# Optimization experiments

Measured on AMD Instinct MI355X. Metric: run time of the kernel, lower is better.

Reference implementation:

```python
import jax, jax.numpy as jnp
import numpy as np
from jax import lax

V, D, L = 32000, 1024, 8
HQ, HKV, HD = 16, 4, 64          # head_dim = D // HQ
H = int(2.6875 * D)              # SwiGLU hidden = 2752
B, S = 2, 1024
WINDOW, GEVERY = 256, 4
EPS, BASE = 1e-6, 10000.0
STD = 0.02


def setup_inputs() -> dict:
    key = jax.random.key(0)
    ks = jax.random.split(key, 10)
    return {
        "idx": jax.random.randint(ks[0], (B, S), 0, V, dtype=jnp.int32),
        "emb": jax.random.normal(ks[1], (V, D), jnp.float32) * STD,
        "Wq": jax.random.normal(ks[2], (L, D, HQ * HD), jnp.float32) * STD,
        "Wk": jax.random.normal(ks[3], (L, D, HKV * HD), jnp.float32) * STD,
        "Wv": jax.random.normal(ks[4], (L, D, HKV * HD), jnp.float32) * STD,
        "Wo": jax.random.normal(ks[5], (L, HQ * HD, D), jnp.float32) * (STD / np.sqrt(2 * L)).astype(np.float32),
        "w1": jax.random.normal(ks[6], (L, D, H), jnp.float32) * STD,
        "w3": jax.random.normal(ks[7], (L, D, H), jnp.float32) * STD,
        "w2": jax.random.normal(ks[8], (L, H, D), jnp.float32) * (STD / np.sqrt(2 * L)).astype(np.float32),
        "n1": jnp.ones((L, D), jnp.float32),
        "n2": jnp.ones((L, D), jnp.float32),
        "nf": jnp.ones((D,), jnp.float32),
    }


def _rmsnorm(x, w):
    return x * lax.rsqrt(jnp.mean(x * x, axis=-1, keepdims=True) + EPS) * w


def _rope(x, cos, sin):
    # x: [B,S,h,HD]; pairs (even, odd) rotated by complex multiply with e^{i*theta}
    x2 = x.reshape(*x.shape[:-1], HD // 2, 2)
    x0, x1 = x2[..., 0], x2[..., 1]
    r0 = x0 * cos - x1 * sin
    r1 = x0 * sin + x1 * cos
    return jnp.stack([r0, r1], axis=-1).reshape(x.shape)


def _forward(idx, emb, Wq, Wk, Wv, Wo, w1, w3, w2, n1, n2, nf):
    # RoPE cache (RoPECache._build_cache)
    inv_freq = 1.0 / (BASE ** (jnp.arange(0, HD, 2, dtype=jnp.float32) / HD))
    t = jnp.arange(S, dtype=jnp.float32)
    freqs = t[:, None] * inv_freq[None, :]                      # [S, HD//2]
    cos = jnp.cos(freqs)[None, :, None, :]                      # [1,S,1,HD//2]
    sin = jnp.sin(freqs)[None, :, None, :]

    # masks: global causal and sliding-window causal (additive, 0 / -inf)
    pos = jnp.arange(S)
    causal = pos[None, :] <= pos[:, None]
    local = causal & ((pos[:, None] - pos[None, :]) < WINDOW)
    neg_inf = jnp.float32(-jnp.inf)
    gmask = jnp.where(causal, 0.0, neg_inf).astype(jnp.float32)
    lmask = jnp.where(local, 0.0, neg_inf).astype(jnp.float32)
    use_global = ((jnp.arange(L) + 1) % GEVERY) == 0            # [L] bool

    scale = 1.0 / (HD ** 0.5)
    rep = HQ // HKV

    def block(x, p):
        wq, wk, wv, wo, W1, W3, W2, g1, g2, ug = p
        h = _rmsnorm(x, g1)
        q = (h @ wq).reshape(B, S, HQ, HD)
        k = (h @ wk).reshape(B, S, HKV, HD)
        v = (h @ wv).reshape(B, S, HKV, HD)
        q = _rope(q, cos, sin)
        k = _rope(k, cos, sin)
        k = jnp.repeat(k, rep, axis=2)                          # GQA: expand KV heads
        v = jnp.repeat(v, rep, axis=2)
        mask = jnp.where(ug, gmask, lmask)
        sc = jnp.einsum('bqhd,bkhd->bhqk', q, k) * scale + mask
        attn = jax.nn.softmax(sc, axis=-1)
        o = jnp.einsum('bhqk,bkhd->bqhd', attn, v).reshape(B, S, HQ * HD)
        x = x + o @ wo
        h2 = _rmsnorm(x, g2)
        x = x + (jax.nn.silu(h2 @ W1) * (h2 @ W3)) @ W2
        return x, None

    x = emb[idx]                                                # token embedding
    x, _ = lax.scan(block, x, (Wq, Wk, Wv, Wo, w1, w3, w2, n1, n2, use_global))
    logits = _rmsnorm(x, nf) @ emb.T                            # tied lm_head
    return logits


def reference(idx, emb, Wq, Wk, Wv, Wo, w1, w3, w2, n1, n2, nf):
    return _forward(idx, emb, Wq, Wk, Wv, Wo, w1, w3, w2, n1, n2, nf)
```

## Files before the change

kernel.cpp:

```cpp
#include <hip/hip_runtime.h>

#define V_ 32000
#define D_ 1024
#define L_ 8
#define HQ_ 16
#define HKV_ 4
#define HD_ 64
#define H_ 2752
#define B_ 2
#define S_ 1024
#define BS_ 2048
#define WINDOW_ 256

typedef float f32x4 __attribute__((ext_vector_type(4)));
typedef short s16x8 __attribute__((ext_vector_type(8)));
typedef unsigned short u16;

__device__ __forceinline__ u16 f2b(float f) {
  union { float f; unsigned u; } a; a.f = f;
  return (u16)((a.u + 0x7fffu + ((a.u >> 16) & 1u)) >> 16);
}
__device__ __forceinline__ float b2f(u16 b) {
  union { unsigned u; float f; } a; a.u = ((unsigned)b) << 16; return a.f;
}

__device__ __forceinline__ void gload_lds16(const void* g, void* l) {
  __builtin_amdgcn_global_load_lds(
      (const __attribute__((address_space(1))) void*)(unsigned long long)(uintptr_t)g,
      (__attribute__((address_space(3))) void*)(unsigned int)(uintptr_t)l,
      16, 0, 0);
}

__global__ void k_cvt(const float* __restrict__ src, u16* __restrict__ dst, long n4) {
  long i = (long)blockIdx.x * blockDim.x + threadIdx.x;
  if (i >= n4) return;
  float4 v = ((const float4*)src)[i];
  ushort4 o; o.x = f2b(v.x); o.y = f2b(v.y); o.z = f2b(v.z); o.w = f2b(v.w);
  ((ushort4*)dst)[i] = o;
}

struct TMat { const float* src; u16* dst; int R, C, t0; };
struct T7 { TMat m[7]; };

__global__ void k_transpose7(T7 P) {
  __shared__ float tile[32][33];
  int bid = blockIdx.x;
  int mi = 0;
#pragma unroll
  for (int i = 1; i < 7; ++i) if (bid >= P.m[i].t0) mi = i;
  TMat mm = P.m[mi];
  int tl = bid - mm.t0;
  int ct = mm.C >> 5;
  int tr = tl / ct, tc = tl - tr * ct;
  int r0 = tr << 5, c0 = tc << 5;
  int tx = threadIdx.x & 31, ty = threadIdx.x >> 5;
#pragma unroll
  for (int j = 0; j < 4; ++j)
    tile[ty + j * 8][tx] = mm.src[(size_t)(r0 + ty + j * 8) * mm.C + c0 + tx];
  __syncthreads();
#pragma unroll
  for (int j = 0; j < 4; ++j)
    mm.dst[(size_t)(c0 + ty + j * 8) * mm.R + r0 + tx] = f2b(tile[tx][ty + j * 8]);
}

__global__ void k_embed(const int* __restrict__ idx, const float* __restrict__ emb,
                        float* __restrict__ x) {
  int t = blockIdx.x;
  int token = idx[t];
  const float4* s = (const float4*)(emb + (size_t)token * D_);
  float4* d = (float4*)(x + (size_t)t * D_);
  d[threadIdx.x] = s[threadIdx.x];
}

__global__ void k_rmsnorm(const float* __restrict__ x, const float* __restrict__ w,
                          u16* __restrict__ out) {
  int row = blockIdx.x, tid = threadIdx.x;
  float4 v = ((const float4*)(x + (size_t)row * D_))[tid];
  float ss = v.x * v.x + v.y * v.y + v.z * v.z + v.w * v.w;
#pragma unroll
  for (int m = 1; m < 64; m <<= 1) ss += __shfl_xor(ss, m, 64);
  __shared__ float red[4];
  if ((tid & 63) == 0) red[tid >> 6] = ss;
  __syncthreads();
  float tot = red[0] + red[1] + red[2] + red[3];
  float rs = rsqrtf(tot * (1.0f / D_) + 1e-6f);
  float4 wv = ((const float4*)w)[tid];
  ushort4 o;
  o.x = f2b(v.x * rs * wv.x); o.y = f2b(v.y * rs * wv.y);
  o.z = f2b(v.z * rs * wv.z); o.w = f2b(v.w * rs * wv.w);
  ((ushort4*)(out + (size_t)row * D_))[tid] = o;
}

__global__ void k_ropetab(float* __restrict__ cosT, float* __restrict__ sinT) {
  int i = blockIdx.x * blockDim.x + threadIdx.x;
  int s = i >> 5, d = i & 31;
  float inv = __expf(-((float)(2 * d) / (float)HD_) * logf(10000.0f));
  float f = (float)s * inv;
  cosT[i] = cosf(f); sinT[i] = sinf(f);
}

__global__ void k_rope(const float* __restrict__ qkvf, const float* __restrict__ cosT,
                       const float* __restrict__ sinT, u16* __restrict__ qh,
                       u16* __restrict__ kh) {
  int t = blockIdx.x;
  int b = t >> 10, s = t & (S_ - 1);
  int tid = threadIdx.x;
  const float* row = qkvf + (size_t)t * 1536;
  for (int p = tid; p < 512; p += 256) {
    int hh = p >> 5, d = p & 31;
    float x0 = row[hh * 64 + 2 * d], x1 = row[hh * 64 + 2 * d + 1];
    float c = cosT[s * 32 + d], sn = sinT[s * 32 + d];
    size_t o = ((size_t)(b * HQ_ + hh) * S_ + s) * HD_ + 2 * d;
    qh[o] = f2b(x0 * c - x1 * sn);
    qh[o + 1] = f2b(x0 * sn + x1 * c);
  }
  if (tid < 128) {
    int hh = tid >> 5, d = tid & 31;
    float x0 = row[1024 + hh * 64 + 2 * d], x1 = row[1024 + hh * 64 + 2 * d + 1];
    float c = cosT[s * 32 + d], sn = sinT[s * 32 + d];
    size_t o = ((size_t)(b * HKV_ + hh) * S_ + s) * HD_ + 2 * d;
    kh[o] = f2b(x0 * c - x1 * sn);
    kh[o + 1] = f2b(x0 * sn + x1 * c);
  }
}

__global__ void k_vtrans(const float* __restrict__ qkvf, u16* __restrict__ vth) {
  __shared__ float tile[32][65];
  const int s0 = blockIdx.x << 5, hh = blockIdx.y, b = blockIdx.z;
  const int tx = threadIdx.x & 63, ty = threadIdx.x >> 6;
#pragma unroll
  for (int j = 0; j < 8; ++j) {
    int sl = j * 4 + ty;
    tile[sl][tx] = qkvf[(size_t)((b << 10) + s0 + sl) * 1536 + 1280 + hh * 64 + tx];
  }
  __syncthreads();
  const int sx = threadIdx.x & 31, dr = threadIdx.x >> 5;
#pragma unroll
  for (int j = 0; j < 8; ++j) {
    int d = j * 8 + dr;
    vth[((size_t)((b * HKV_ + hh) << 6) + d) * S_ + s0 + sx] = f2b(tile[sx][d]);
  }
}

template <int EPI>
__global__ __launch_bounds__(256) void k_gemm(const u16* __restrict__ A,
                                              const u16* __restrict__ BT,
                                              void* __restrict__ Cp, int M, int N, int K,
                                              int ldc) {
  (void)M; (void)N;
  __shared__ u16 As[3][4096];
  __shared__ u16 Bs[3][4096];
  const int tid = threadIdx.x;
  const int lane = tid & 63, wid = tid >> 6;
  const int lin = blockIdx.y * 16 + blockIdx.x;
  const int cpx = (gridDim.x * gridDim.y) >> 3;
  const int swz = (lin & 7) * cpx + (lin >> 3);
  const int m0 = (swz & 15) << 7, n0 = (swz >> 4) << 7;
  const int wm = (wid >> 1) << 6, wn = (wid & 1) << 6;
  const int fr = lane & 15, fg = lane >> 4;

  f32x4 acc[4][4] = {};

  const int srow = (wid << 4) + (lane >> 2);
  const int scol = ((lane & 3) - ((lane >> 3) & 3)) & 3;
  const u16* ga = A + (size_t)(m0 + srow) * K + (scol << 3);
  const u16* gb = BT + (size_t)(n0 + srow) * K + (scol << 3);
  const int cb = wid << 9;

  auto stage = [&](int buf, int k0) {
    u16* la = &As[buf][cb];
    u16* lb = &Bs[buf][cb];
    gload_lds16(ga + k0, la);
    gload_lds16(ga + (size_t)64 * K + k0, la + 2048);
    gload_lds16(gb + k0, lb);
    gload_lds16(gb + (size_t)64 * K + k0, lb + 2048);
  };

  const int nk = K >> 5;
  stage(0, 0);
  stage(1, 32);

  const int ab = (wid >> 1) << 2, bb = (wid & 1) << 2;
  const int foff = (fr << 5) + ((((fg + (fr >> 1)) & 3)) << 3);
  int cur = 0;
  for (int t = 0; t < nk; ++t) {
    if (t + 2 < nk) {
      int nb = cur + 2; if (nb >= 3) nb -= 3;
      stage(nb, (t + 2) << 5);
      asm volatile("s_waitcnt vmcnt(8)" ::: "memory");
    } else if (t + 2 == nk) {
      asm volatile("s_waitcnt vmcnt(4)" ::: "memory");
    } else {
      asm volatile("s_waitcnt vmcnt(0)" ::: "memory");
    }
    __builtin_amdgcn_s_barrier();
    s16x8 af[4], bq[4];
#pragma unroll
    for (int i = 0; i < 4; ++i) {
      af[i] = *(const s16x8*)(&As[cur][((ab + i) << 9) + foff]);
      bq[i] = *(const s16x8*)(&Bs[cur][((bb + i) << 9) + foff]);
    }
#pragma unroll
    for (int mi = 0; mi < 4; ++mi)
#pragma unroll
      for (int ni = 0; ni < 4; ++ni)
        acc[mi][ni] = __builtin_amdgcn_mfma_f32_16x16x32_bf16(af[mi], bq[ni], acc[mi][ni], 0, 0, 0);
    __builtin_amdgcn_s_barrier();
    if (++cur == 3) cur = 0;
  }

#pragma unroll
  for (int mi = 0; mi < 4; ++mi) {
#pragma unroll
    for (int ni = 0; ni < 4; ++ni) {
#pragma unroll
      for (int r = 0; r < 4; ++r) {
        int row = m0 + wm + mi * 16 + fg * 4 + r;
        int col = n0 + wn + ni * 16 + fr;
        size_t off = (size_t)row * ldc + col;
        float v = acc[mi][ni][r];
        if (EPI == 0) ((float*)Cp)[off] = v;
        else if (EPI == 1) ((float*)Cp)[off] += v;
        else ((u16*)Cp)[off] = f2b(v);
      }
    }
  }
}

template <int EPI>
__global__ __launch_bounds__(256, 2) void k_gemm2(const u16* __restrict__ A,
                                                  const u16* __restrict__ BT,
                                                  void* __restrict__ Cp, int K, int ldc) {
  __shared__ u16 As[3][8192];
  __shared__ u16 Bs[3][4096];
  const int tid = threadIdx.x;
  const int lane = tid & 63, wid = tid >> 6;
  const int lin = blockIdx.y * gridDim.x + blockIdx.x;
  const int cpx = (gridDim.x * gridDim.y) >> 3;
  const int swz = (lin & 7) * cpx + (lin >> 3);
  const int m0 = (swz & 7) << 8, n0 = (swz >> 3) << 7;
  const int fr = lane & 15, fg = lane >> 4;

  f32x4 acc[4][8] = {};

  const int srow = lane >> 2;
  const int scol = ((lane & 3) - ((lane >> 3) & 3)) & 3;
  const u16* ga = A + (size_t)(m0 + (wid << 6) + srow) * K + (scol << 3);
  const u16* gb = BT + (size_t)(n0 + (wid << 5) + srow) * K + (scol << 3);
  const int cba = wid << 11;
  const int cbb = wid << 10;

  auto stage = [&](int buf, int k0) {
    u16* la = &As[buf][cba];
    u16* lb = &Bs[buf][cbb];
    gload_lds16(ga + k0, la);
    gload_lds16(ga + (size_t)16 * K + k0, la + 512);
    gload_lds16(ga + (size_t)32 * K + k0, la + 1024);
    gload_lds16(ga + (size_t)48 * K + k0, la + 1536);
    gload_lds16(gb + k0, lb);
    gload_lds16(gb + (size_t)16 * K + k0, lb + 512);
  };

  const int nk = K >> 5;
  stage(0, 0);
  stage(1, 32);

  const int foff = (fr << 5) + ((((fg + (fr >> 1)) & 3)) << 3);
  int cur = 0;
  for (int t = 0; t < nk; ++t) {
    if (t + 2 < nk) {
      int nb = cur + 2; if (nb >= 3) nb -= 3;
      stage(nb, (t + 2) << 5);
      asm volatile("s_waitcnt vmcnt(12)" ::: "memory");
    } else if (t + 2 == nk) {
      asm volatile("s_waitcnt vmcnt(6)" ::: "memory");
    } else {
      asm volatile("s_waitcnt vmcnt(0)" ::: "memory");
    }
    __builtin_amdgcn_s_barrier();
    s16x8 af[4], bq[8];
#pragma unroll
    for (int i = 0; i < 4; ++i)
      af[i] = *(const s16x8*)(&As[cur][(((wid << 2) + i) << 9) + foff]);
#pragma unroll
    for (int j = 0; j < 8; ++j)
      bq[j] = *(const s16x8*)(&Bs[cur][(j << 9) + foff]);
#pragma unroll
    for (int mi = 0; mi < 4; ++mi)
#pragma unroll
      for (int ni = 0; ni < 8; ++ni)
        acc[mi][ni] = __builtin_amdgcn_mfma_f32_16x16x32_bf16(af[mi], bq[ni], acc[mi][ni], 0, 0, 0);
    __builtin_amdgcn_s_barrier();
    if (++cur == 3) cur = 0;
  }

#pragma unroll
  for (int mi = 0; mi < 4; ++mi) {
#pragma unroll
    for (int ni = 0; ni < 8; ++ni) {
#pragma unroll
      for (int r = 0; r < 4; ++r) {
        int row = m0 + (wid << 6) + mi * 16 + fg * 4 + r;
        int col = n0 + ni * 16 + fr;
        size_t off = (size_t)row * ldc + col;
        float v = acc[mi][ni][r];
        if (EPI == 0) ((float*)Cp)[off] = v;
        else if (EPI == 1) ((float*)Cp)[off] += v;
        else ((u16*)Cp)[off] = f2b(v);
      }
    }
  }
}

__global__ __launch_bounds__(256) void k_attn(const u16* __restrict__ qh,
                                              const u16* __restrict__ kh,
                                              const u16* __restrict__ vth,
                                              u16* __restrict__ attno, int isGlobal) {
  __shared__ u16 pb[4][512];
  const int qblk = blockIdx.x, hq = blockIdx.y, b = blockIdx.z;
  const int lane = threadIdx.x & 63, wid = threadIdx.x >> 6;
  const int fr = lane & 15, fg = lane >> 4;
  const int q0 = (qblk << 6) + (wid << 4);
  const int hk = hq >> 2;
  const u16* Q = qh + ((size_t)(b * HQ_ + hq) * S_) * HD_;
  const u16* Kh = kh + ((size_t)(b * HKV_ + hk) * S_) * HD_;
  const u16* VT = vth + ((size_t)(b * HKV_ + hk) * HD_) * S_;
  u16* pbuf = pb[wid];

  const s16x8 aq0 = *(const s16x8*)(Q + (q0 + fr) * HD_ + fg * 8);
  const s16x8 aq1 = *(const s16x8*)(Q + (q0 + fr) * HD_ + 32 + fg * 8);

  f32x4 o0 = {}, o1 = {}, o2 = {}, o3 = {};
  float m[4], l[4];
#pragma unroll
  for (int r = 0; r < 4; ++r) { m[r] = -1e30f; l[r] = 0.0f; }

  int kt0 = 0;
  if (!isGlobal) { int lo = q0 - (WINDOW_ - 1); if (lo > 0) kt0 = lo & ~31; }
  const int ktend = q0 + 16;

  for (int kt = kt0; kt < ktend; kt += 32) {
    f32x4 sc0 = {}, sc1 = {};
    {
      s16x8 b0 = *(const s16x8*)(Kh + (kt + fr) * HD_ + fg * 8);
      s16x8 b1 = *(const s16x8*)(Kh + (kt + fr) * HD_ + 32 + fg * 8);
      sc0 = __builtin_amdgcn_mfma_f32_16x16x32_bf16(aq0, b0, sc0, 0, 0, 0);
      sc0 = __builtin_amdgcn_mfma_f32_16x16x32_bf16(aq1, b1, sc0, 0, 0, 0);
      s16x8 c0 = *(const s16x8*)(Kh + (kt + 16 + fr) * HD_ + fg * 8);
      s16x8 c1 = *(const s16x8*)(Kh + (kt + 16 + fr) * HD_ + 32 + fg * 8);
      sc1 = __builtin_amdgcn_mfma_f32_16x16x32_bf16(aq0, c0, sc1, 0, 0, 0);
      sc1 = __builtin_amdgcn_mfma_f32_16x16x32_bf16(aq1, c1, sc1, 0, 0, 0);
    }
#pragma unroll
    for (int r = 0; r < 4; ++r) {
      int row = q0 + fg * 4 + r;
      int col0 = kt + fr, col1 = kt + 16 + fr;
      bool v0 = (col0 <= row) && (isGlobal || (row - col0) < WINDOW_);
      bool v1 = (col1 <= row) && (isGlobal || (row - col1) < WINDOW_);
      float s0 = v0 ? sc0[r] * 0.125f : -1e30f;
      float s1 = v1 ? sc1[r] * 0.125f : -1e30f;
      float t = fmaxf(s0, s1);
#pragma unroll
      for (int msk = 1; msk < 16; msk <<= 1) t = fmaxf(t, __shfl_xor(t, msk, 16));
      float mn = fmaxf(m[r], t);
      float fsc = __expf(m[r] - mn);
      m[r] = mn;
      float p0 = v0 ? __expf(s0 - mn) : 0.0f;
      float p1 = v1 ? __expf(s1 - mn) : 0.0f;
      float ps = p0 + p1;
#pragma unroll
      for (int msk = 1; msk < 16; msk <<= 1) ps += __shfl_xor(ps, msk, 16);
      l[r] = l[r] * fsc + ps;
      o0[r] *= fsc; o1[r] *= fsc; o2[r] *= fsc; o3[r] *= fsc;
      pbuf[(fg * 4 + r) * 32 + fr] = f2b(p0);
      pbuf[(fg * 4 + r) * 32 + 16 + fr] = f2b(p1);
    }
    s16x8 ap = *(const s16x8*)(pbuf + fr * 32 + fg * 8);
    {
      s16x8 bv0 = *(const s16x8*)(VT + (size_t)(0 + fr) * S_ + kt + fg * 8);
      o0 = __builtin_amdgcn_mfma_f32_16x16x32_bf16(ap, bv0, o0, 0, 0, 0);
      s16x8 bv1 = *(const s16x8*)(VT + (size_t)(16 + fr) * S_ + kt + fg * 8);
      o1 = __builtin_amdgcn_mfma_f32_16x16x32_bf16(ap, bv1, o1, 0, 0, 0);
      s16x8 bv2 = *(const s16x8*)(VT + (size_t)(32 + fr) * S_ + kt + fg * 8);
      o2 = __builtin_amdgcn_mfma_f32_16x16x32_bf16(ap, bv2, o2, 0, 0, 0);
      s16x8 bv3 = *(const s16x8*)(VT + (size_t)(48 + fr) * S_ + kt + fg * 8);
      o3 = __builtin_amdgcn_mfma_f32_16x16x32_bf16(ap, bv3, o3, 0, 0, 0);
    }
  }

#pragma unroll
  for (int r = 0; r < 4; ++r) {
    int row = q0 + fg * 4 + r;
    float inv = 1.0f / l[r];
    size_t base = ((size_t)b * S_ + row) * (HQ_ * HD_) + hq * HD_;
    attno[base + fr] = f2b(o0[r] * inv);
    attno[base + 16 + fr] = f2b(o1[r] * inv);
    attno[base + 32 + fr] = f2b(o2[r] * inv);
    attno[base + 48 + fr] = f2b(o3[r] * inv);
  }
}

__global__ void k_silu(const u16* __restrict__ h13, u16* __restrict__ g) {
  long c = (long)blockIdx.x * 256 + threadIdx.x;
  int t = (int)(c / 688);
  int j = (int)(c - (long)t * 688) * 4;
  const u16* a = h13 + (size_t)t * 5504 + j;
  ushort4 av = *(const ushort4*)a;
  ushort4 bv = *(const ushort4*)(a + 2752);
  ushort4 ov;
  {
    float x0 = b2f(av.x), y0 = b2f(bv.x);
    ov.x = f2b(x0 / (1.0f + __expf(-x0)) * y0);
  }
  {
    float x0 = b2f(av.y), y0 = b2f(bv.y);
    ov.y = f2b(x0 / (1.0f + __expf(-x0)) * y0);
  }
  {
    float x0 = b2f(av.z), y0 = b2f(bv.z);
    ov.z = f2b(x0 / (1.0f + __expf(-x0)) * y0);
  }
  {
    float x0 = b2f(av.w), y0 = b2f(bv.w);
    ov.w = f2b(x0 / (1.0f + __expf(-x0)) * y0);
  }
  *(ushort4*)(g + (size_t)t * 2752 + j) = ov;
}

extern "C" void kernel_launch(void* const* d_in, const int* in_sizes, int n_in,
                              void* d_out, int out_size, void* d_ws, size_t ws_size,
                              hipStream_t stream) {
  (void)in_sizes; (void)n_in; (void)out_size; (void)ws_size;
  const int* idx = (const int*)d_in[0];
  const float* emb = (const float*)d_in[1];
  const float* Wq = (const float*)d_in[2];
  const float* Wk = (const float*)d_in[3];
  const float* Wv = (const float*)d_in[4];
  const float* Wo = (const float*)d_in[5];
  const float* w1 = (const float*)d_in[6];
  const float* w3 = (const float*)d_in[7];
  const float* w2 = (const float*)d_in[8];
  const float* n1 = (const float*)d_in[9];
  const float* n2 = (const float*)d_in[10];
  const float* nf = (const float*)d_in[11];
  float* out = (float*)d_out;

  char* p = (char*)d_ws;
  auto carve = [&](size_t bytes) {
    char* q = p;
    p += (bytes + 255) & ~(size_t)255;
    return (void*)q;
  };
  float* x = (float*)carve((size_t)BS_ * D_ * 4);
  u16* h = (u16*)carve((size_t)BS_ * D_ * 2);
  float* qkvf = (float*)carve((size_t)BS_ * 1536 * 4);
  u16* qh = (u16*)carve((size_t)B_ * HQ_ * S_ * HD_ * 2);
  u16* khb = (u16*)carve((size_t)B_ * HKV_ * S_ * HD_ * 2);
  u16* vth = (u16*)carve((size_t)B_ * HKV_ * HD_ * S_ * 2);
  u16* attno = (u16*)carve((size_t)BS_ * D_ * 2);
  u16* h13 = (u16*)carve((size_t)BS_ * 5504 * 2);
  u16* g = (u16*)carve((size_t)BS_ * H_ * 2);
  u16* wT = (u16*)carve((size_t)11075584 * 2);
  float* cosT = (float*)carve((size_t)S_ * 32 * 4);
  float* sinT = (float*)carve((size_t)S_ * 32 * 4);
  u16* embb = (u16*)carve((size_t)V_ * D_ * 2);

  k_cvt<<<V_ * D_ / 4 / 256, 256, 0, stream>>>(emb, embb, (long)V_ * D_ / 4);
  k_ropetab<<<S_ * 32 / 256, 256, 0, stream>>>(cosT, sinT);
  k_embed<<<BS_, 256, 0, stream>>>(idx, emb, x);

  for (int l = 0; l < L_; ++l) {
    T7 t7;
    t7.m[0] = { Wq + (size_t)l * D_ * 1024, wT, D_, 1024, 0 };
    t7.m[1] = { Wk + (size_t)l * D_ * 256, wT + 1048576, D_, 256, 1024 };
    t7.m[2] = { Wv + (size_t)l * D_ * 256, wT + 1310720, D_, 256, 1280 };
    t7.m[3] = { Wo + (size_t)l * 1024 * D_, wT + 1572864, 1024, D_, 1536 };
    t7.m[4] = { w1 + (size_t)l * D_ * H_, wT + 2621440, D_, H_, 2560 };
    t7.m[5] = { w3 + (size_t)l * D_ * H_, wT + 5439488, D_, H_, 5312 };
    t7.m[6] = { w2 + (size_t)l * H_ * D_, wT + 8257536, H_, D_, 8064 };
    k_transpose7<<<10816, 256, 0, stream>>>(t7);

    k_rmsnorm<<<BS_, 256, 0, stream>>>(x, n1 + (size_t)l * D_, h);
    k_gemm<0><<<dim3(16, 12), 256, 0, stream>>>(h, wT, qkvf, BS_, 1536, 1024, 1536);
    k_rope<<<BS_, 256, 0, stream>>>(qkvf, cosT, sinT, qh, khb);
    k_vtrans<<<dim3(32, HKV_, B_), 256, 0, stream>>>(qkvf, vth);
    int ig = ((l + 1) % 4) == 0;
    k_attn<<<dim3(16, HQ_, B_), 256, 0, stream>>>(qh, khb, vth, attno, ig);
    k_gemm<1><<<dim3(16, 8), 256, 0, stream>>>(attno, wT + 1572864, x, BS_, 1024, 1024, 1024);
    k_rmsnorm<<<BS_, 256, 0, stream>>>(x, n2 + (size_t)l * D_, h);
    k_gemm2<2><<<dim3(8, 43), 256, 0, stream>>>(h, wT + 2621440, h13, 1024, 5504);
    k_silu<<<BS_ * 688 / 256, 256, 0, stream>>>(h13, g);
    k_gemm<1><<<dim3(16, 8), 256, 0, stream>>>(g, wT + 8257536, x, BS_, 1024, 2752, 1024);
  }

  k_rmsnorm<<<BS_, 256, 0, stream>>>(x, nf, h);
  k_gemm2<0><<<dim3(8, 250), 256, 0, stream>>>(h, embb, out, 1024, 32000);
}
```

Before: 1.631 ms.

## Fuse SiLU gating into W1/W3 GEMM epilogue and split-K residual GEMMs with atomics

The W1 and W3 weights are now interleaved row by row during the transpose, so each adjacent column pair of the fused GEMM output is (gate, up). The GEMM epilogue combines each pair with a lane shuffle and writes the SiLU product directly to g. This removes the h13 buffer and the separate k_silu kernel. The Wo and W2 GEMMs are split along K into two z-slices that accumulate into x with atomicAdd, doubling the block count at the cost of atomic traffic and non-deterministic summation order.

```diff
diff --git a/kernel.cpp b/kernel.cpp
--- a/kernel.cpp
+++ b/kernel.cpp
@@ -39,7 +39,7 @@
   ((ushort4*)dst)[i] = o;
 }
 
-struct TMat { const float* src; u16* dst; int R, C, t0; };
+struct TMat { const float* src; u16* dst; int R, C, t0, mul, add; };
 struct T7 { TMat m[7]; };
 
 __global__ void k_transpose7(T7 P) {
@@ -60,7 +60,8 @@
   __syncthreads();
 #pragma unroll
   for (int j = 0; j < 4; ++j)
-    mm.dst[(size_t)(c0 + ty + j * 8) * mm.R + r0 + tx] = f2b(tile[tx][ty + j * 8]);
+    mm.dst[((size_t)(c0 + ty + j * 8) * mm.mul + mm.add) * mm.R + r0 + tx] =
+        f2b(tile[tx][ty + j * 8]);
 }
 
 __global__ void k_embed(const int* __restrict__ idx, const float* __restrict__ emb,
@@ -145,9 +146,8 @@
 template <int EPI>
 __global__ __launch_bounds__(256) void k_gemm(const u16* __restrict__ A,
                                               const u16* __restrict__ BT,
-                                              void* __restrict__ Cp, int M, int N, int K,
-                                              int ldc) {
-  (void)M; (void)N;
+                                              void* __restrict__ Cp, int kdepth,
+                                              int lda, int ldc) {
   __shared__ u16 As[3][4096];
   __shared__ u16 Bs[3][4096];
   const int tid = threadIdx.x;
@@ -163,20 +163,21 @@
 
   const int srow = (wid << 4) + (lane >> 2);
   const int scol = ((lane & 3) - ((lane >> 3) & 3)) & 3;
-  const u16* ga = A + (size_t)(m0 + srow) * K + (scol << 3);
-  const u16* gb = BT + (size_t)(n0 + srow) * K + (scol << 3);
+  const int kz = blockIdx.z * kdepth;
+  const u16* ga = A + (size_t)(m0 + srow) * lda + kz + (scol << 3);
+  const u16* gb = BT + (size_t)(n0 + srow) * lda + kz + (scol << 3);
   const int cb = wid << 9;
 
   auto stage = [&](int buf, int k0) {
     u16* la = &As[buf][cb];
     u16* lb = &Bs[buf][cb];
     gload_lds16(ga + k0, la);
-    gload_lds16(ga + (size_t)64 * K + k0, la + 2048);
+    gload_lds16(ga + (size_t)64 * lda + k0, la + 2048);
     gload_lds16(gb + k0, lb);
-    gload_lds16(gb + (size_t)64 * K + k0, lb + 2048);
+    gload_lds16(gb + (size_t)64 * lda + k0, lb + 2048);
   };
 
-  const int nk = K >> 5;
+  const int nk = kdepth >> 5;
   stage(0, 0);
   stage(1, 32);
 
@@ -220,8 +221,7 @@
         size_t off = (size_t)row * ldc + col;
         float v = acc[mi][ni][r];
         if (EPI == 0) ((float*)Cp)[off] = v;
-        else if (EPI == 1) ((float*)Cp)[off] += v;
-        else ((u16*)Cp)[off] = f2b(v);
+        else atomicAdd((float*)Cp + off, v);
       }
     }
   }
@@ -302,11 +302,16 @@
       for (int r = 0; r < 4; ++r) {
         int row = m0 + (wid << 6) + mi * 16 + fg * 4 + r;
         int col = n0 + ni * 16 + fr;
-        size_t off = (size_t)row * ldc + col;
         float v = acc[mi][ni][r];
-        if (EPI == 0) ((float*)Cp)[off] = v;
-        else if (EPI == 1) ((float*)Cp)[off] += v;
-        else ((u16*)Cp)[off] = f2b(v);
+        if (EPI == 0) {
+          ((float*)Cp)[(size_t)row * ldc + col] = v;
+        } else {
+          float o = __shfl_xor(v, 1, 64);
+          if (!(fr & 1)) {
+            float s = v / (1.0f + __expf(-v)) * o;
+            ((u16*)Cp)[(size_t)row * ldc + (col >> 1)] = f2b(s);
+          }
+        }
       }
     }
   }
@@ -398,33 +403,6 @@
     attno[base + 32 + fr] = f2b(o2[r] * inv);
     attno[base + 48 + fr] = f2b(o3[r] * inv);
   }
-}
-
-__global__ void k_silu(const u16* __restrict__ h13, u16* __restrict__ g) {
-  long c = (long)blockIdx.x * 256 + threadIdx.x;
-  int t = (int)(c / 688);
-  int j = (int)(c - (long)t * 688) * 4;
-  const u16* a = h13 + (size_t)t * 5504 + j;
-  ushort4 av = *(const ushort4*)a;
-  ushort4 bv = *(const ushort4*)(a + 2752);
-  ushort4 ov;
-  {
-    float x0 = b2f(av.x), y0 = b2f(bv.x);
-    ov.x = f2b(x0 / (1.0f + __expf(-x0)) * y0);
-  }
-  {
-    float x0 = b2f(av.y), y0 = b2f(bv.y);
-    ov.y = f2b(x0 / (1.0f + __expf(-x0)) * y0);
-  }
-  {
-    float x0 = b2f(av.z), y0 = b2f(bv.z);
-    ov.z = f2b(x0 / (1.0f + __expf(-x0)) * y0);
-  }
-  {
-    float x0 = b2f(av.w), y0 = b2f(bv.w);
-    ov.w = f2b(x0 / (1.0f + __expf(-x0)) * y0);
-  }
-  *(ushort4*)(g + (size_t)t * 2752 + j) = ov;
 }
 
 extern "C" void kernel_launch(void* const* d_in, const int* in_sizes, int n_in,
@@ -458,7 +436,6 @@
   u16* khb = (u16*)carve((size_t)B_ * HKV_ * S_ * HD_ * 2);
   u16* vth = (u16*)carve((size_t)B_ * HKV_ * HD_ * S_ * 2);
   u16* attno = (u16*)carve((size_t)BS_ * D_ * 2);
-  u16* h13 = (u16*)carve((size_t)BS_ * 5504 * 2);
   u16* g = (u16*)carve((size_t)BS_ * H_ * 2);
   u16* wT = (u16*)carve((size_t)11075584 * 2);
   float* cosT = (float*)carve((size_t)S_ * 32 * 4);
@@ -471,26 +448,25 @@
 
   for (int l = 0; l < L_; ++l) {
     T7 t7;
-    t7.m[0] = { Wq + (size_t)l * D_ * 1024, wT, D_, 1024, 0 };
-    t7.m[1] = { Wk + (size_t)l * D_ * 256, wT + 1048576, D_, 256, 1024 };
-    t7.m[2] = { Wv + (size_t)l * D_ * 256, wT + 1310720, D_, 256, 1280 };
-    t7.m[3] = { Wo + (size_t)l * 1024 * D_, wT + 1572864, 1024, D_, 1536 };
-    t7.m[4] = { w1 + (size_t)l * D_ * H_, wT + 2621440, D_, H_, 2560 };
-    t7.m[5] = { w3 + (size_t)l * D_ * H_, wT + 5439488, D_, H_, 5312 };
-    t7.m[6] = { w2 + (size_t)l * H_ * D_, wT + 8257536, H_, D_, 8064 };
+    t7.m[0] = { Wq + (size_t)l * D_ * 1024, wT, D_, 1024, 0, 1, 0 };
+    t7.m[1] = { Wk + (size_t)l * D_ * 256, wT + 1048576, D_, 256, 1024, 1, 0 };
+    t7.m[2] = { Wv + (size_t)l * D_ * 256, wT + 1310720, D_, 256, 1280, 1, 0 };
+    t7.m[3] = { Wo + (size_t)l * 1024 * D_, wT + 1572864, 1024, D_, 1536, 1, 0 };
+    t7.m[4] = { w1 + (size_t)l * D_ * H_, wT + 2621440, D_, H_, 2560, 2, 0 };
+    t7.m[5] = { w3 + (size_t)l * D_ * H_, wT + 2621440, D_, H_, 5312, 2, 1 };
+    t7.m[6] = { w2 + (size_t)l * H_ * D_, wT + 8257536, H_, D_, 8064, 1, 0 };
     k_transpose7<<<10816, 256, 0, stream>>>(t7);
 
     k_rmsnorm<<<BS_, 256, 0, stream>>>(x, n1 + (size_t)l * D_, h);
-    k_gemm<0><<<dim3(16, 12), 256, 0, stream>>>(h, wT, qkvf, BS_, 1536, 1024, 1536);
+    k_gemm<0><<<dim3(16, 12), 256, 0, stream>>>(h, wT, qkvf, 1024, 1024, 1536);
     k_rope<<<BS_, 256, 0, stream>>>(qkvf, cosT, sinT, qh, khb);
     k_vtrans<<<dim3(32, HKV_, B_), 256, 0, stream>>>(qkvf, vth);
     int ig = ((l + 1) % 4) == 0;
     k_attn<<<dim3(16, HQ_, B_), 256, 0, stream>>>(qh, khb, vth, attno, ig);
-    k_gemm<1><<<dim3(16, 8), 256, 0, stream>>>(attno, wT + 1572864, x, BS_, 1024, 1024, 1024);
+    k_gemm<4><<<dim3(16, 8, 2), 256, 0, stream>>>(attno, wT + 1572864, x, 512, 1024, 1024);
     k_rmsnorm<<<BS_, 256, 0, stream>>>(x, n2 + (size_t)l * D_, h);
-    k_gemm2<2><<<dim3(8, 43), 256, 0, stream>>>(h, wT + 2621440, h13, 1024, 5504);
-    k_silu<<<BS_ * 688 / 256, 256, 0, stream>>>(h13, g);
-    k_gemm<1><<<dim3(16, 8), 256, 0, stream>>>(g, wT + 8257536, x, BS_, 1024, 2752, 1024);
+    k_gemm2<3><<<dim3(8, 43), 256, 0, stream>>>(h, wT + 2621440, g, 1024, 2752);
+    k_gemm<4><<<dim3(16, 8, 2), 256, 0, stream>>>(g, wT + 8257536, x, 1376, 2752, 1024);
   }
 
   k_rmsnorm<<<BS_, 256, 0, stream>>>(x, nf, h);
```

Measured after the change: 1.520 ms. -6.8%, faster.
